# Performance work log

Hardware: AMD Instinct MI355X
Metric: run time of the kernel (lower is better)

The kernel has to match this reference:

```python
import jax, jax.numpy as jnp
import numpy as np

K = 36  # neighbors

def _gather(points, idx):
    # points: [B,N,C], idx: [B,N,K] -> [B,N,K,C]
    return jax.vmap(lambda p, i: p[i])(points, idx)

def setup_inputs() -> dict:
    key = jax.random.key(0)
    ks = jax.random.split(key, 16)
    B, N, d_points, d_model = 4, 4096, 32, 128
    def lin(k, fan_in, shape):
        return jax.random.normal(k, shape, dtype=jnp.float32) / np.sqrt(fan_in)
    return {
        "features": jax.random.normal(ks[0], (B, N, d_points), dtype=jnp.float32),
        "xyz": jax.random.uniform(ks[1], (B, N, 3), dtype=jnp.float32),
        "W1": lin(ks[2], d_points, (d_model, d_points)), "b1": jnp.zeros((d_model,), jnp.float32),
        "W2": lin(ks[3], d_model, (d_model, d_model)), "b2": jnp.zeros((d_model,), jnp.float32),
        "Wd1": lin(ks[4], 3, (d_model, 3)), "bd1": jnp.zeros((d_model,), jnp.float32),
        "Wd2": lin(ks[5], d_model, (d_model, d_model)), "bd2": jnp.zeros((d_model,), jnp.float32),
        "Wg1": lin(ks[6], d_model, (d_model, d_model)), "bg1": jnp.zeros((d_model,), jnp.float32),
        "Wg2": lin(ks[7], d_model, (d_model, d_model)), "bg2": jnp.zeros((d_model,), jnp.float32),
    }

def reference(features, xyz, W1, b1, W2, b2, Wd1, bd1, Wd2, bd2, Wg1, bg1, Wg2, bg2):
    # square_distance: [B,N,N]
    sq = jnp.sum(xyz * xyz, axis=-1)
    dists = sq[:, :, None] + sq[:, None, :] - 2.0 * jnp.einsum('bnc,bmc->bnm', xyz, xyz)
    knn_idx = jnp.argsort(dists, axis=-1)[:, :, :K]            # [B,N,K]
    knn_xyz = _gather(xyz, knn_idx)                             # [B,N,K,3]
    x = features @ W1.T + b1                                    # [B,N,d]
    k = _gather(x, knn_idx)                                     # [B,N,K,d]
    v = k
    # fc_delta(xyz[:,:,None] - knn_xyz)
    d_in = xyz[:, :, None, :] - knn_xyz                         # [B,N,K,3]
    pos_enc = jax.nn.relu(d_in @ Wd1.T + bd1) @ Wd2.T + bd2     # [B,N,K,d]
    # fc_gamma(q[:,:,None] - k + pos_enc)
    g_in = x[:, :, None, :] - k + pos_enc
    attn_pre = jax.nn.relu(g_in @ Wg1.T + bg1) @ Wg2.T + bg2    # [B,N,K,d]
    attn = jax.nn.softmax(attn_pre / np.sqrt(x.shape[-1]).astype(np.float32), axis=-2)
    res = jnp.einsum('bmnf,bmnf->bmf', attn, v + pos_enc)       # [B,N,d]
    res = res @ W2.T + b2 + x
    return (res, attn)
```

## Files before the change

kernel.cpp:

```cpp
#include <hip/hip_runtime.h>
#include <math.h>

#define BB 4
#define NPT 4096
#define DP 32
#define DD 128
#define KNB 36

typedef unsigned short ushort_t;
typedef unsigned int uint_t;
typedef unsigned long long ull;
typedef __attribute__((ext_vector_type(8))) short bf16x8;
typedef __attribute__((ext_vector_type(4))) float f32x4;
typedef __attribute__((ext_vector_type(4))) uint_t u32x4;

__device__ __forceinline__ ushort_t f2bf(float f) {
    unsigned u = __float_as_uint(f);
    unsigned r = (u + 0x7FFFu + ((u >> 16) & 1u)) >> 16;
    return (ushort_t)r;
}
__device__ __forceinline__ uint_t cvtpk(float lo, float hi) {
    uint_t r;
    asm("v_cvt_pk_bf16_f32 %0, %1, %2" : "=v"(r) : "v"(lo), "v"(hi));
    return r;
}
__device__ __forceinline__ ushort_t f2bf1(float f) { return (ushort_t)cvtpk(f, f); }
__device__ __forceinline__ float bf2f(ushort_t h) {
    return __uint_as_float((unsigned)h << 16);
}
__device__ __forceinline__ int swzi(int r, int f) {
    return (r << 7) + (((f >> 3) ^ (r & 15)) << 3) + (f & 7);
}

__global__ __launch_bounds__(256) void k_wcvt(const float* __restrict__ Wd2,
                                              const float* __restrict__ Wg1,
                                              const float* __restrict__ Wg2,
                                              const float* __restrict__ W2,
                                              ushort_t* __restrict__ wb) {
    int i = blockIdx.x * 256 + threadIdx.x;
    wb[i]           = f2bf(Wd2[i]);
    wb[i + 16384]   = f2bf(Wg1[i]);
    wb[i + 32768]   = f2bf(Wg2[i]);
    wb[i + 49152]   = f2bf(W2[i]);
}

__global__ __launch_bounds__(128) void k_x(const float* __restrict__ feat,
                                           const float* __restrict__ xyz,
                                           const float* __restrict__ W1,
                                           const float* __restrict__ b1,
                                           float* __restrict__ x,
                                           float* __restrict__ sq) {
    int row = blockIdx.x;
    int t = threadIdx.x;
    __shared__ float sf[DP];
    if (t < DP) sf[t] = feat[row * DP + t];
    __syncthreads();
    float acc = 0.f;
#pragma unroll
    for (int c = 0; c < DP; ++c) acc = fmaf(sf[c], W1[t * DP + c], acc);
    x[(size_t)row * DD + t] = acc + b1[t];
    if (t == 0) {
        float a = xyz[row * 3 + 0], b = xyz[row * 3 + 1], c = xyz[row * 3 + 2];
        float s = __fadd_rn(__fadd_rn(__fmul_rn(a, a), __fmul_rn(b, b)),
                            __fmul_rn(c, c));
        sq[row] = s;
    }
}

__global__ __launch_bounds__(256) void k_knn2(const float* __restrict__ xyz,
                                              const float* __restrict__ sq,
                                              int* __restrict__ knn) {
    const int row = blockIdx.x;
    const int b = row >> 12;
    const int t = threadIdx.x;
    const int lane = t & 63, wv = t >> 6;

    __shared__ __align__(16) ull cand[2048];
    __shared__ int wsum[4];
    __shared__ ull wred[4];
    __shared__ ull sbest;
    __shared__ int sC, sCnt;

    uint_t* hist4 = (uint_t*)cand;

    const float qx = xyz[row * 3 + 0], qy = xyz[row * 3 + 1], qz = xyz[row * 3 + 2];
    const float qs = sq[row];
    const float* bx = xyz + (size_t)b * NPT * 3;
    const float* bs = sq + (size_t)b * NPT;

#pragma unroll
    for (int i = 0; i < 16; ++i) hist4[t + (i << 8)] = 0;
    if (t == 0) sCnt = 0;
    __syncthreads();

    uint_t k16[16];
#pragma unroll
    for (int i = 0; i < 16; ++i) {
        int m = t + (i << 8);
        float px = bx[m * 3 + 0], py = bx[m * 3 + 1], pz = bx[m * 3 + 2];
        float d0 = __fmul_rn(qx, px);
        float d1 = __fmaf_rn(qy, py, d0);
        float dot = __fmaf_rn(qz, pz, d1);
        float d = __fsub_rn(__fadd_rn(qs, bs[m]), __fmul_rn(2.0f, dot));
        unsigned u = __float_as_uint(d);
        u = (u & 0x80000000u) ? ~u : (u | 0x80000000u);
        k16[i] = u;
        int bin = (u < 0x80000000u) ? 0 : (int)((u - 0x80000000u) >> 21);
        atomicAdd(&hist4[(bin << 2) | (t & 3)], 1u);
    }
    __syncthreads();

    int s_t = 0;
#pragma unroll
    for (int i = 0; i < 16; ++i) s_t += (int)hist4[(t << 4) + i];
    int v = s_t;
    for (int off = 1; off < 64; off <<= 1) {
        int o = __shfl_up(v, off, 64);
        if (lane >= off) v += o;
    }
    if (lane == 63) wsum[wv] = v;
    __syncthreads();
    int base = 0;
    for (int w0 = 0; w0 < wv; ++w0) base += wsum[w0];
    int cumIncl = base + v, cumExcl = cumIncl - s_t;
    if (cumExcl < KNB && cumIncl >= KNB) {
        int run = cumExcl;
#pragma unroll
        for (int j = 0; j < 4; ++j) {
            int bb = (t << 2) + j;
            int h = (int)(hist4[(bb << 2) + 0] + hist4[(bb << 2) + 1] +
                          hist4[(bb << 2) + 2] + hist4[(bb << 2) + 3]);
            if (run + h >= KNB) { sC = bb; break; }
            run += h;
        }
    }
    __syncthreads();
    const int C = sC;

#pragma unroll
    for (int i = 0; i < 16; ++i) {
        uint_t u = k16[i];
        int bin = (u < 0x80000000u) ? 0 : (int)((u - 0x80000000u) >> 21);
        if (bin <= C) {
            int p = atomicAdd(&sCnt, 1);
            if (p < 2048) cand[p] = ((ull)u << 32) | (uint_t)(t + (i << 8));
        }
    }
    __syncthreads();
    const int cnt = sCnt;

    if (cnt <= 64) {
        if (wv == 0) {
            ull x = (lane < cnt) ? cand[lane] : ~0ull;
#pragma unroll
            for (int k = 2; k <= 64; k <<= 1) {
#pragma unroll
                for (int j = k >> 1; j > 0; j >>= 1) {
                    ull o = __shfl_xor(x, j, 64);
                    bool up = ((lane & k) == 0);
                    bool lower = ((lane & j) == 0);
                    ull mn = (x < o) ? x : o;
                    ull mx = (x < o) ? o : x;
                    x = (up == lower) ? mn : mx;
                }
            }
            if (lane < KNB) knn[(size_t)row * KNB + lane] = (int)(x & 0xffffffffu);
        }
        return;
    }

    if (cnt <= 2048) {
        ull lk = ~0ull;
        for (int i = t; i < cnt; i += 256) { ull k = cand[i]; if (k < lk) lk = k; }
        for (int r = 0; r < KNB; ++r) {
            ull k = lk;
#pragma unroll
            for (int off = 32; off >= 1; off >>= 1) {
                ull o = __shfl_down(k, off, 64);
                if (o < k) k = o;
            }
            if (lane == 0) wred[wv] = k;
            __syncthreads();
            if (t == 0) {
                ull best = wred[0];
                for (int w0 = 1; w0 < 4; ++w0) if (wred[w0] < best) best = wred[w0];
                sbest = best;
                knn[(size_t)row * KNB + r] = (int)(best & 0xffffffffu);
            }
            __syncthreads();
            ull best = sbest;
            if (lk == best) {
                for (int i = t; i < cnt; i += 256)
                    if (cand[i] == best) cand[i] = ~0ull;
                ull nm = ~0ull;
                for (int i = t; i < cnt; i += 256) { ull kk = cand[i]; if (kk < nm) nm = kk; }
                lk = nm;
            }
        }
        return;
    }

    {
        uint_t* bm = (uint_t*)cand;
        if (t < 128) bm[t] = 0;
        __syncthreads();
        ull lk = ~0ull;
#pragma unroll
        for (int i = 0; i < 16; ++i) {
            ull k = ((ull)k16[i] << 32) | (uint_t)(t + (i << 8));
            if (k < lk) lk = k;
        }
        for (int r = 0; r < KNB; ++r) {
            ull k = lk;
#pragma unroll
            for (int off = 32; off >= 1; off >>= 1) {
                ull o = __shfl_down(k, off, 64);
                if (o < k) k = o;
            }
            if (lane == 0) wred[wv] = k;
            __syncthreads();
            if (t == 0) {
                ull best = wred[0];
                for (int w0 = 1; w0 < 4; ++w0) if (wred[w0] < best) best = wred[w0];
                sbest = best;
                knn[(size_t)row * KNB + r] = (int)(best & 0xffffffffu);
            }
            __syncthreads();
            ull best = sbest;
            int bi = (int)(best & 0xffffffffu);
            if ((bi & 255) == t) {
                bm[bi >> 5] |= (1u << (bi & 31));
                ull nm = ~0ull;
#pragma unroll
                for (int i = 0; i < 16; ++i) {
                    int m = t + (i << 8);
                    if ((bm[m >> 5] >> (m & 31)) & 1u) continue;
                    ull kk = ((ull)k16[i] << 32) | (uint_t)m;
                    if (kk < nm) nm = kk;
                }
                lk = nm;
            }
        }
    }
}

__global__ __launch_bounds__(256) void k_fused2(
    const float* __restrict__ xyz, const float* __restrict__ x,
    const int* __restrict__ knn,
    const float* __restrict__ Wd1, const float* __restrict__ bd1,
    const float* __restrict__ bd2, const float* __restrict__ bg1,
    const float* __restrict__ bg2, const float* __restrict__ b2,
    const ushort_t* __restrict__ Wd2b, const ushort_t* __restrict__ Wg1b,
    const ushort_t* __restrict__ Wg2b, const ushort_t* __restrict__ W2b,
    float* __restrict__ out_res, float* __restrict__ out_attn) {

    const int p0 = blockIdx.x * 2;
    const int b = p0 >> 12;
    const int t = threadIdx.x;
    const int w = t >> 6;
    const int l = t & 63;
    const int q4 = l >> 4;

    __shared__ __align__(16) ushort_t Abuf[72 * 128];
    __shared__ __align__(16) ushort_t Vbuf[72 * 128];
    __shared__ int sidxb[72];
    __shared__ float dxb[72 * 3];
    __shared__ float Wd1s[384];
    __shared__ float bd1s[128];

    const int c0 = ((w * 2) << 4) + (l & 15);
    const int c1 = c0 + 16;
    float xn_r[2][2];
#pragma unroll
    for (int g = 0; g < 2; ++g) {
        xn_r[0][g] = x[(size_t)(p0 + g) * DD + c0];
        xn_r[1][g] = x[(size_t)(p0 + g) * DD + c1];
    }
    const float bd2_r[2] = {bd2[c0], bd2[c1]};
    const float bg1_r[2] = {bg1[c0], bg1[c1]};
    const float bg2_r[2] = {bg2[c0], bg2[c1]};
    const float b2_r[2]  = {b2[c0],  b2[c1]};

    if (t < 72) sidxb[t] = knn[(size_t)p0 * KNB + t];
    if (t >= 72 && t < 200) bd1s[t - 72] = bd1[t - 72];
    if (t >= 128 && t < 128 + 96) {
        int i = t - 128;
        reinterpret_cast<float4*>(Wd1s)[i] = reinterpret_cast<const float4*>(Wd1)[i];
    }
    __syncthreads();

    if (t < 72) {
        int g = (t >= KNB);
        int j = sidxb[t];
#pragma unroll
        for (int c = 0; c < 3; ++c)
            dxb[t * 3 + c] = xyz[(size_t)(p0 + g) * 3 + c] - xyz[((size_t)(b << 12) + j) * 3 + c];
    }
    for (int e = t; e < 72 * 16; e += 256) {
        int r = e >> 4, cb = e & 15;
        const float4* xr = reinterpret_cast<const float4*>(x + ((size_t)(b << 12) + sidxb[r]) * DD);
        float4 a0 = xr[cb * 2], a1 = xr[cb * 2 + 1];
        u32x4 pk = {cvtpk(a0.x, a0.y), cvtpk(a0.z, a0.w),
                    cvtpk(a1.x, a1.y), cvtpk(a1.z, a1.w)};
        *reinterpret_cast<u32x4*>(&Vbuf[(r << 7) + (cb << 3)]) = pk;
    }
    __syncthreads();

    for (int e = t; e < 72 * 16; e += 256) {
        int r = e >> 4, cb = e & 15;
        float dx0 = dxb[r * 3 + 0], dx1 = dxb[r * 3 + 1], dx2 = dxb[r * 3 + 2];
        float v[8];
#pragma unroll
        for (int u = 0; u < 8; ++u) {
            int f = (cb << 3) + u;
            v[u] = fmaxf(fmaf(Wd1s[f * 3 + 0], dx0,
                         fmaf(Wd1s[f * 3 + 1], dx1,
                              Wd1s[f * 3 + 2] * dx2)) + bd1s[f], 0.f);
        }
        u32x4 pk = {cvtpk(v[0], v[1]), cvtpk(v[2], v[3]),
                    cvtpk(v[4], v[5]), cvtpk(v[6], v[7])};
        *reinterpret_cast<u32x4*>(&Abuf[(r << 7) + ((cb ^ (r & 15)) << 3)]) = pk;
    }
    __syncthreads();

    const f32x4 z4 = {0.f, 0.f, 0.f, 0.f};

    auto run_gemm = [&](const ushort_t* Wb, f32x4 acc[5][2]) {
        bf16x8 bfrag[2][4];
#pragma unroll
        for (int n2 = 0; n2 < 2; ++n2)
#pragma unroll
            for (int kt = 0; kt < 4; ++kt) {
                int f = ((w * 2 + n2) << 4) + (l & 15);
                int k = (kt << 5) + ((l >> 4) << 3);
                bfrag[n2][kt] = *reinterpret_cast<const bf16x8*>(Wb + f * 128 + k);
            }
        __builtin_amdgcn_s_setprio(1);
#pragma unroll
        for (int mt = 0; mt < 5; ++mt) {
#pragma unroll
            for (int kt = 0; kt < 4; ++kt) {
                int r = (mt << 4) + (l & 15);
                int cs = ((kt << 2) + (l >> 4)) ^ (l & 15);
                bf16x8 a = *reinterpret_cast<const bf16x8*>(&Abuf[(r << 7) + (cs << 3)]);
                acc[mt][0] = __builtin_amdgcn_mfma_f32_16x16x32_bf16(a, bfrag[0][kt], acc[mt][0], 0, 0, 0);
                acc[mt][1] = __builtin_amdgcn_mfma_f32_16x16x32_bf16(a, bfrag[1][kt], acc[mt][1], 0, 0, 0);
            }
        }
        __builtin_amdgcn_s_setprio(0);
    };

    {
        f32x4 acc[5][2];
#pragma unroll
        for (int mt = 0; mt < 5; ++mt) { acc[mt][0] = z4; acc[mt][1] = z4; }
        run_gemm(Wd2b, acc);
        __syncthreads();
#pragma unroll
        for (int mt = 0; mt < 5; ++mt) {
            int row0 = (mt << 4) + (q4 << 2);
            if (row0 < 72) {
                int g = (row0 >= KNB);
#pragma unroll
                for (int n2 = 0; n2 < 2; ++n2) {
                    int col = (n2 == 0) ? c0 : c1;
                    float xn_sel = xn_r[n2][g];
#pragma unroll
                    for (int rr = 0; rr < 4; ++rr) {
                        int row = row0 + rr;
                        int vs = (row << 7) + col;
                        float pe = acc[mt][n2][rr] + bd2_r[n2];
                        float xk = bf2f(Vbuf[vs]);
                        Vbuf[vs] = f2bf1(xk + pe);
                        float gin = (xn_sel - xk) + pe;
                        Abuf[swzi(row, col)] = f2bf1(gin);
                    }
                }
            }
        }
        __syncthreads();
    }

    {
        f32x4 acc[5][2];
#pragma unroll
        for (int mt = 0; mt < 5; ++mt) { acc[mt][0] = z4; acc[mt][1] = z4; }
        run_gemm(Wg1b, acc);
        __syncthreads();
#pragma unroll
        for (int mt = 0; mt < 5; ++mt) {
            int row0 = (mt << 4) + (q4 << 2);
            if (row0 < 72) {
#pragma unroll
                for (int n2 = 0; n2 < 2; ++n2) {
                    int col = (n2 == 0) ? c0 : c1;
#pragma unroll
                    for (int rr = 0; rr < 4; ++rr)
                        Abuf[swzi(row0 + rr, col)] = f2bf1(fmaxf(acc[mt][n2][rr] + bg1_r[n2], 0.f));
                }
            }
        }
        __syncthreads();
    }

    {
        f32x4 acc[5][2];
#pragma unroll
        for (int mt = 0; mt < 5; ++mt) { acc[mt][0] = z4; acc[mt][1] = z4; }
        run_gemm(Wg2b, acc);
        __syncthreads();
#pragma unroll
        for (int mt = 0; mt < 5; ++mt) {
            int row0 = (mt << 4) + (q4 << 2);
            if (row0 < 72) {
#pragma unroll
                for (int n2 = 0; n2 < 2; ++n2) {
                    int col = (n2 == 0) ? c0 : c1;
#pragma unroll
                    for (int rr = 0; rr < 4; ++rr)
                        Abuf[((row0 + rr) << 7) + col] = f2bf1(acc[mt][n2][rr] + bg2_r[n2]);
                }
            }
        }
        __syncthreads();
    }

    const float sc = 0.08838834764831845f;
    float ra;
    {
        int g = t >> 7, f = t & 127;
        const ushort_t* sbase = Abuf + (g * KNB << 7) + f;
        const ushort_t* vbase = Vbuf + (g * KNB << 7) + f;
        float p[KNB];
        float m = -__builtin_inff();
#pragma unroll
        for (int kk = 0; kk < KNB; ++kk) {
            p[kk] = bf2f(sbase[kk << 7]);
            m = fmaxf(m, p[kk]);
        }
        float sum = 0.f;
#pragma unroll
        for (int kk = 0; kk < KNB; ++kk) {
            float e_ = __expf((p[kk] - m) * sc);
            p[kk] = e_;
            sum += e_;
        }
        float inv = 1.f / sum;
        ra = 0.f;
        float* obase = out_attn + ((size_t)(p0 + g) * KNB) * DD + f;
#pragma unroll
        for (int kk = 0; kk < KNB; ++kk) {
            float a_ = p[kk] * inv;
            obase[(size_t)kk * DD] = a_;
            ra = fmaf(a_, bf2f(vbase[kk << 7]), ra);
        }
    }
    __syncthreads();
    {
        int g = t >> 7, f = t & 127;
        Abuf[swzi(g, f)] = f2bf1(ra);
    }
    __syncthreads();

    {
        f32x4 acc0 = z4, acc1 = z4;
#pragma unroll
        for (int kt = 0; kt < 4; ++kt) {
            int r = (l & 15);
            int cs = ((kt << 2) + (l >> 4)) ^ (l & 15);
            bf16x8 a = *reinterpret_cast<const bf16x8*>(&Abuf[(r << 7) + (cs << 3)]);
            int k = (kt << 5) + ((l >> 4) << 3);
            bf16x8 b0 = *reinterpret_cast<const bf16x8*>(W2b + c0 * 128 + k);
            bf16x8 b1 = *reinterpret_cast<const bf16x8*>(W2b + c1 * 128 + k);
            acc0 = __builtin_amdgcn_mfma_f32_16x16x32_bf16(a, b0, acc0, 0, 0, 0);
            acc1 = __builtin_amdgcn_mfma_f32_16x16x32_bf16(a, b1, acc1, 0, 0, 0);
        }
        if ((l >> 4) == 0) {
#pragma unroll
            for (int rr = 0; rr < 2; ++rr) {
                out_res[(size_t)(p0 + rr) * DD + c0] = acc0[rr] + b2_r[0] + xn_r[0][rr];
                out_res[(size_t)(p0 + rr) * DD + c1] = acc1[rr] + b2_r[1] + xn_r[1][rr];
            }
        }
    }
}

extern "C" void kernel_launch(void* const* d_in, const int* in_sizes, int n_in,
                              void* d_out, int out_size, void* d_ws, size_t ws_size,
                              hipStream_t stream) {
    const float* feat = (const float*)d_in[0];
    const float* xyz = (const float*)d_in[1];
    const float* W1 = (const float*)d_in[2];
    const float* b1 = (const float*)d_in[3];
    const float* W2 = (const float*)d_in[4];
    const float* b2 = (const float*)d_in[5];
    const float* Wd1 = (const float*)d_in[6];
    const float* bd1 = (const float*)d_in[7];
    const float* Wd2 = (const float*)d_in[8];
    const float* bd2 = (const float*)d_in[9];
    const float* Wg1 = (const float*)d_in[10];
    const float* bg1 = (const float*)d_in[11];
    const float* Wg2 = (const float*)d_in[12];
    const float* bg2 = (const float*)d_in[13];

    float* out = (float*)d_out;
    float* out_res = out;
    float* out_attn = out + (size_t)BB * NPT * DD;

    float* ws_x = (float*)d_ws;
    float* ws_sq = ws_x + (size_t)BB * NPT * DD;
    int* ws_idx = (int*)(ws_sq + (size_t)BB * NPT);
    ushort_t* wb = (ushort_t*)(ws_idx + (size_t)BB * NPT * KNB);
    ushort_t* Wd2b = wb;
    ushort_t* Wg1b = wb + 16384;
    ushort_t* Wg2b = wb + 32768;
    ushort_t* W2b = wb + 49152;

    hipLaunchKernelGGL(k_wcvt, dim3(64), dim3(256), 0, stream, Wd2, Wg1, Wg2, W2, wb);
    hipLaunchKernelGGL(k_x, dim3(BB * NPT), dim3(128), 0, stream,
                       feat, xyz, W1, b1, ws_x, ws_sq);
    hipLaunchKernelGGL(k_knn2, dim3(BB * NPT), dim3(256), 0, stream,
                       xyz, ws_sq, ws_idx);
    hipLaunchKernelGGL(k_fused2, dim3(BB * NPT / 2), dim3(256), 0, stream,
                       xyz, ws_x, ws_idx, Wd1, bd1, bd2, bg1, bg2, b2,
                       Wd2b, Wg1b, Wg2b, W2b, out_res, out_attn);
}
```

Measured before the change: 338.6 us.

## Fuse softmax and weighted sum into Wg2 GEMM epilogue registers

Computes the softmax over neighbors directly on the MFMA accumulators of the final gamma GEMM. Row max, sum and the attention-weighted reduction are done with cross-lane shuffles instead of writing logits to LDS and re-reading them per feature thread. The v+pos_enc values are kept packed as bf16 in registers rather than written back to LDS. This removes LDS round trips and a synchronization, at the cost of more registers and strided 4-row attn stores per lane.

```diff
diff --git a/kernel.cpp b/kernel.cpp
--- a/kernel.cpp
+++ b/kernel.cpp
@@ -28,6 +28,8 @@
 __device__ __forceinline__ float bf2f(ushort_t h) {
     return __uint_as_float((unsigned)h << 16);
 }
+__device__ __forceinline__ float pk_lo(uint_t u) { return __uint_as_float(u << 16); }
+__device__ __forceinline__ float pk_hi(uint_t u) { return __uint_as_float(u & 0xFFFF0000u); }
 __device__ __forceinline__ int swzi(int r, int f) {
     return (r << 7) + (((f >> 3) ^ (r & 15)) << 3) + (f & 7);
 }
@@ -350,6 +352,8 @@
         __builtin_amdgcn_s_setprio(0);
     };
 
+    uint_t vpe_pk[5][2][2];
+
     {
         f32x4 acc[5][2];
 #pragma unroll
@@ -365,16 +369,23 @@
                 for (int n2 = 0; n2 < 2; ++n2) {
                     int col = (n2 == 0) ? c0 : c1;
                     float xn_sel = xn_r[n2][g];
+                    float vp[4];
 #pragma unroll
                     for (int rr = 0; rr < 4; ++rr) {
                         int row = row0 + rr;
-                        int vs = (row << 7) + col;
                         float pe = acc[mt][n2][rr] + bd2_r[n2];
-                        float xk = bf2f(Vbuf[vs]);
-                        Vbuf[vs] = f2bf1(xk + pe);
+                        float xk = bf2f(Vbuf[(row << 7) + col]);
+                        vp[rr] = xk + pe;
                         float gin = (xn_sel - xk) + pe;
                         Abuf[swzi(row, col)] = f2bf1(gin);
                     }
+                    vpe_pk[mt][n2][0] = cvtpk(vp[0], vp[1]);
+                    vpe_pk[mt][n2][1] = cvtpk(vp[2], vp[3]);
+                }
+            } else {
+#pragma unroll
+                for (int n2 = 0; n2 < 2; ++n2) {
+                    vpe_pk[mt][n2][0] = 0; vpe_pk[mt][n2][1] = 0;
                 }
             }
         }
@@ -403,62 +414,112 @@
         __syncthreads();
     }
 
+    const float sc = 0.08838834764831845f;
+    const float NI = -__builtin_inff();
+    float ra0[2], ra1[2];
     {
         f32x4 acc[5][2];
 #pragma unroll
         for (int mt = 0; mt < 5; ++mt) { acc[mt][0] = z4; acc[mt][1] = z4; }
         run_gemm(Wg2b, acc);
-        __syncthreads();
+
+        float m0[2] = {NI, NI}, m1[2] = {NI, NI};
 #pragma unroll
         for (int mt = 0; mt < 5; ++mt) {
             int row0 = (mt << 4) + (q4 << 2);
             if (row0 < 72) {
+                bool hi = (row0 >= KNB);
+#pragma unroll
+                for (int n2 = 0; n2 < 2; ++n2) {
+                    acc[mt][n2][0] += bg2_r[n2]; acc[mt][n2][1] += bg2_r[n2];
+                    acc[mt][n2][2] += bg2_r[n2]; acc[mt][n2][3] += bg2_r[n2];
+                    float v = fmaxf(fmaxf(acc[mt][n2][0], acc[mt][n2][1]),
+                                    fmaxf(acc[mt][n2][2], acc[mt][n2][3]));
+                    m0[n2] = fmaxf(m0[n2], hi ? NI : v);
+                    m1[n2] = fmaxf(m1[n2], hi ? v : NI);
+                }
+            }
+        }
+#pragma unroll
+        for (int n2 = 0; n2 < 2; ++n2) {
+            m0[n2] = fmaxf(m0[n2], __shfl_xor(m0[n2], 16, 64));
+            m0[n2] = fmaxf(m0[n2], __shfl_xor(m0[n2], 32, 64));
+            m1[n2] = fmaxf(m1[n2], __shfl_xor(m1[n2], 16, 64));
+            m1[n2] = fmaxf(m1[n2], __shfl_xor(m1[n2], 32, 64));
+        }
+
+        float s0[2] = {0.f, 0.f}, s1[2] = {0.f, 0.f};
+#pragma unroll
+        for (int mt = 0; mt < 5; ++mt) {
+            int row0 = (mt << 4) + (q4 << 2);
+            if (row0 < 72) {
+                bool hi = (row0 >= KNB);
+#pragma unroll
+                for (int n2 = 0; n2 < 2; ++n2) {
+                    float mm = hi ? m1[n2] : m0[n2];
+                    float sl = 0.f;
+#pragma unroll
+                    for (int rr = 0; rr < 4; ++rr) {
+                        float p = __expf((acc[mt][n2][rr] - mm) * sc);
+                        acc[mt][n2][rr] = p;
+                        sl += p;
+                    }
+                    s0[n2] += hi ? 0.f : sl;
+                    s1[n2] += hi ? sl : 0.f;
+                }
+            }
+        }
+        float i0[2], i1[2];
+#pragma unroll
+        for (int n2 = 0; n2 < 2; ++n2) {
+            float v0 = s0[n2];
+            v0 += __shfl_xor(v0, 16, 64); v0 += __shfl_xor(v0, 32, 64);
+            i0[n2] = 1.f / v0;
+            float v1 = s1[n2];
+            v1 += __shfl_xor(v1, 16, 64); v1 += __shfl_xor(v1, 32, 64);
+            i1[n2] = 1.f / v1;
+        }
+
+        ra0[0] = ra0[1] = ra1[0] = ra1[1] = 0.f;
+#pragma unroll
+        for (int mt = 0; mt < 5; ++mt) {
+            int row0 = (mt << 4) + (q4 << 2);
+            if (row0 < 72) {
+                bool hi = (row0 >= KNB);
 #pragma unroll
                 for (int n2 = 0; n2 < 2; ++n2) {
                     int col = (n2 == 0) ? c0 : c1;
-#pragma unroll
-                    for (int rr = 0; rr < 4; ++rr)
-                        Abuf[((row0 + rr) << 7) + col] = f2bf1(acc[mt][n2][rr] + bg2_r[n2]);
-                }
-            }
-        }
-        __syncthreads();
-    }
-
-    const float sc = 0.08838834764831845f;
-    float ra;
-    {
-        int g = t >> 7, f = t & 127;
-        const ushort_t* sbase = Abuf + (g * KNB << 7) + f;
-        const ushort_t* vbase = Vbuf + (g * KNB << 7) + f;
-        float p[KNB];
-        float m = -__builtin_inff();
-#pragma unroll
-        for (int kk = 0; kk < KNB; ++kk) {
-            p[kk] = bf2f(sbase[kk << 7]);
-            m = fmaxf(m, p[kk]);
-        }
-        float sum = 0.f;
-#pragma unroll
-        for (int kk = 0; kk < KNB; ++kk) {
-            float e_ = __expf((p[kk] - m) * sc);
-            p[kk] = e_;
-            sum += e_;
-        }
-        float inv = 1.f / sum;
-        ra = 0.f;
-        float* obase = out_attn + ((size_t)(p0 + g) * KNB) * DD + f;
-#pragma unroll
-        for (int kk = 0; kk < KNB; ++kk) {
-            float a_ = p[kk] * inv;
-            obase[(size_t)kk * DD] = a_;
-            ra = fmaf(a_, bf2f(vbase[kk << 7]), ra);
-        }
-    }
-    __syncthreads();
-    {
-        int g = t >> 7, f = t & 127;
-        Abuf[swzi(g, f)] = f2bf1(ra);
+                    float iv = hi ? i1[n2] : i0[n2];
+                    float* ob = out_attn + ((size_t)p0 * KNB + row0) * DD + col;
+                    float v0 = pk_lo(vpe_pk[mt][n2][0]), v1 = pk_hi(vpe_pk[mt][n2][0]);
+                    float v2 = pk_lo(vpe_pk[mt][n2][1]), v3 = pk_hi(vpe_pk[mt][n2][1]);
+                    float a0 = acc[mt][n2][0] * iv, a1 = acc[mt][n2][1] * iv;
+                    float a2 = acc[mt][n2][2] * iv, a3 = acc[mt][n2][3] * iv;
+                    ob[0]      = a0;
+                    ob[DD]     = a1;
+                    ob[2 * DD] = a2;
+                    ob[3 * DD] = a3;
+                    float dloc = fmaf(a0, v0, fmaf(a1, v1, fmaf(a2, v2, a3 * v3)));
+                    ra0[n2] += hi ? 0.f : dloc;
+                    ra1[n2] += hi ? dloc : 0.f;
+                }
+            }
+        }
+#pragma unroll
+        for (int n2 = 0; n2 < 2; ++n2) {
+            ra0[n2] += __shfl_xor(ra0[n2], 16, 64);
+            ra0[n2] += __shfl_xor(ra0[n2], 32, 64);
+            ra1[n2] += __shfl_xor(ra1[n2], 16, 64);
+            ra1[n2] += __shfl_xor(ra1[n2], 32, 64);
+        }
+    }
+    __syncthreads();
+
+    if (q4 == 0) {
+        Abuf[swzi(0, c0)] = f2bf1(ra0[0]);
+        Abuf[swzi(0, c1)] = f2bf1(ra0[1]);
+        Abuf[swzi(1, c0)] = f2bf1(ra1[0]);
+        Abuf[swzi(1, c1)] = f2bf1(ra1[1]);
     }
     __syncthreads();
 
```

After: 371.2 us. 1.1x slower.
